# Optimization experiments

Measured on AMD Instinct MI355X. Metric: run time of the kernel, lower is better.

The kernel has to match this reference:

```python
import jax, jax.numpy as jnp
import numpy as np

NUM_JOINTS = 140
NUM_VERTICES = 13059
NUM_BONES = 28
BATCH = 512


def euler_zyx_to_rot(e):
    """e: [..., 3] Euler angles in (z, y, x) order -> [..., 3, 3] with R = Rz @ Ry @ Rx."""
    z, y, x = e[..., 0], e[..., 1], e[..., 2]
    cx, sx = jnp.cos(x), jnp.sin(x)
    cy, sy = jnp.cos(y), jnp.sin(y)
    cz, sz = jnp.cos(z), jnp.sin(z)
    r00 = cz * cy
    r01 = cz * sy * sx - sz * cx
    r02 = cz * sy * cx + sz * sx
    r10 = sz * cy
    r11 = sz * sy * sx + cz * cx
    r12 = sz * sy * cx - cz * sx
    r20 = -sy
    r21 = cy * sx
    r22 = cy * cx
    R = jnp.stack([r00, r01, r02, r10, r11, r12, r20, r21, r22], axis=-1)
    return R.reshape(e.shape[:-1] + (3, 3))


def _mouse_forward(pose, bone_lengths, center_bone_length, trans, scale,
                   v_template, t_pose_joints, weights, parent, bone_mapper):
    B = pose.shape[0]
    Jn = NUM_JOINTS
    dt = pose.dtype

    bl = jax.nn.sigmoid(bone_lengths / 5.0) * 2.0            # [B, 28]
    R = euler_zyx_to_rot(pose.reshape(B, Jn, 3))             # [B, J, 3, 3]
    Jt = t_pose_joints                                       # [J, 3]

    # bone offsets for joints 1..J-1, scaled per bone_length_mapper
    off = Jt[1:] - Jt[parent[1:]]                            # [J-1, 3]
    blid = bone_mapper[1:]                                   # [J-1]
    bl_g = jnp.where(blid[None, :] >= 0,
                     jnp.take(bl, jnp.maximum(blid, 0), axis=1),
                     jnp.ones((), dt))                       # [B, J-1]
    # joint index 1 (position 0 in the [J-1] arrays) uses center_bone_length
    scale_per = bl_g.at[:, 0].set(center_bone_length[:, 0])
    off_b = off[None] * scale_per[..., None]                 # [B, J-1, 3]

    bottom = jnp.broadcast_to(jnp.array([0., 0., 0., 1.], dt), (B, Jn - 1, 1, 4))
    top = jnp.concatenate([R[:, 1:], off_b[..., None]], axis=-1)   # [B, J-1, 3, 4]
    A = jnp.concatenate([top, bottom], axis=-2)              # [B, J-1, 4, 4] local transforms

    root_t = jnp.broadcast_to(Jt[0], (B, 3))[..., None]      # [B, 3, 1]
    root_top = jnp.concatenate([R[:, 0], root_t], axis=-1)   # [B, 3, 4]
    root_bot = jnp.broadcast_to(jnp.array([0., 0., 0., 1.], dt), (B, 1, 4))
    G0 = jnp.concatenate([root_top, root_bot], axis=-2)      # [B, 4, 4]

    G_init = jnp.zeros((B, Jn, 4, 4), dt).at[:, 0].set(G0)

    def step(G, xs):
        i, p, Ai = xs                                        # Ai: [B, 4, 4]
        Gp = jnp.take(G, p, axis=1)                          # [B, 4, 4]
        Gi = Gp @ Ai
        return G.at[:, i].set(Gi), None

    idx = jnp.arange(1, Jn)
    G, _ = jax.lax.scan(step, G_init, (idx, parent[1:], jnp.swapaxes(A, 0, 1)))

    J_final = G[:, :, :3, 3]                                 # [B, J, 3]

    # subtract rest-pose joint contribution (relative transforms for LBS)
    Jh = jnp.concatenate([jnp.broadcast_to(Jt, (B, Jn, 3)),
                          jnp.zeros((B, Jn, 1), dt)], axis=-1)      # [B, J, 4]
    d = jnp.einsum('bjmn,bjn->bjm', G, Jh)                   # [B, J, 4]
    G_rel = jnp.concatenate([G[..., :3], (G[..., 3] - d)[..., None]], axis=-1)

    # linear blend skinning
    T = jnp.einsum('vj,bjmn->bvmn', weights, G_rel)          # [B, V, 4, 4]
    vh = jnp.concatenate([v_template, jnp.ones((NUM_VERTICES, 1), dt)], axis=-1)
    V = jnp.einsum('bvmn,vn->bvm', T[:, :, :3, :], vh)       # [B, V, 3]

    s = scale[:, 0][:, None, None]
    V = V * s + trans[:, None, :]
    J_out = J_final * s + trans[:, None, :]
    return V, J_out


def setup_inputs() -> dict:
    key = jax.random.key(0)
    ks = jax.random.split(key, 8)
    rng = np.random.default_rng(0)
    parent = np.zeros(NUM_JOINTS, dtype=np.int32)
    for i in range(1, NUM_JOINTS):
        parent[i] = rng.integers(0, i)                       # valid kinematic tree
    bone_mapper = rng.integers(-1, NUM_BONES, size=NUM_JOINTS).astype(np.int32)
    W = jax.random.uniform(ks[6], (NUM_VERTICES, NUM_JOINTS), jnp.float32)
    W = W / jnp.sum(W, axis=1, keepdims=True)                # row-stochastic skinning weights
    return {
        'pose': jax.random.normal(ks[0], (BATCH, NUM_JOINTS * 3), jnp.float32) * 0.2,
        'bone_lengths': jax.random.normal(ks[1], (BATCH, NUM_BONES), jnp.float32),
        'center_bone_length': jax.random.uniform(ks[2], (BATCH, 1), jnp.float32, 0.5, 1.5),
        'trans': jax.random.normal(ks[3], (BATCH, 3), jnp.float32),
        'scale': jax.random.uniform(ks[4], (BATCH, 1), jnp.float32, 0.5, 1.5),
        'v_template': jax.random.normal(ks[5], (NUM_VERTICES, 3), jnp.float32),
        't_pose_joints': jax.random.normal(ks[7], (NUM_JOINTS, 3), jnp.float32),
        'weights': W,
        'parent': jnp.asarray(parent),
        'bone_mapper': jnp.asarray(bone_mapper),
    }


def reference(pose, bone_lengths, center_bone_length, trans, scale,
              v_template, t_pose_joints, weights, parent, bone_mapper):
    return _mouse_forward(pose, bone_lengths, center_bone_length, trans, scale,
                          v_template, t_pose_joints, weights, parent, bone_mapper)
```

## Files before the change

kernel.cpp:

```cpp
#include <hip/hip_runtime.h>
#include <math.h>

#define NJ 140
#define NV 13059
#define NB 512
#define NBONES 28

#define MTILES 103
#define NBLK 12
#define KS 18
#define GRID_GEMM (MTILES*NBLK)

#define APREP_SLOTS (MTILES*KS*512)

typedef _Float16 f16x8 __attribute__((ext_vector_type(8)));
typedef float    f32x4 __attribute__((ext_vector_type(4)));

#define GL16(gp, lp) __builtin_amdgcn_global_load_lds( \
    (const __attribute__((address_space(1))) unsigned int*)(gp), \
    (__attribute__((address_space(3))) unsigned int*)(lp), 16, 0, 0)

__global__ __launch_bounds__(256) void kin_kernel(
    const float* __restrict__ pose,
    const float* __restrict__ bone_lengths,
    const float* __restrict__ cbl,
    const float* __restrict__ trans,
    const float* __restrict__ scale,
    const float* __restrict__ t_pose,
    const int*   __restrict__ parent,
    const int*   __restrict__ bone_mapper,
    _Float16* __restrict__ Bp,
    float* __restrict__ jout)
{
    const int t = threadIdx.x;

    __shared__ float M0[NJ][12];
    __shared__ float M1[NJ][12];
    __shared__ int   a0[NJ];
    __shared__ int   a1[NJ];

    const int b = blockIdx.x;

    if (t < NJ) {
        const int j = t;
        float z = pose[b*(NJ*3) + 3*j + 0];
        float y = pose[b*(NJ*3) + 3*j + 1];
        float x = pose[b*(NJ*3) + 3*j + 2];
        float cx = cosf(x), sx = sinf(x);
        float cy = cosf(y), sy = sinf(y);
        float cz = cosf(z), sz = sinf(z);
        float r00 = cz*cy;
        float r01 = cz*sy*sx - sz*cx;
        float r02 = cz*sy*cx + sz*sx;
        float r10 = sz*cy;
        float r11 = sz*sy*sx + cz*cx;
        float r12 = sz*sy*cx - cz*sx;
        float r20 = -sy;
        float r21 = cy*sx;
        float r22 = cy*cx;
        float t0, t1, t2;
        int p = parent[j];
        if (j == 0) {
            t0 = t_pose[0]; t1 = t_pose[1]; t2 = t_pose[2];
        } else {
            float ox = t_pose[3*j+0] - t_pose[3*p+0];
            float oy = t_pose[3*j+1] - t_pose[3*p+1];
            float oz = t_pose[3*j+2] - t_pose[3*p+2];
            float s;
            if (j == 1) {
                s = cbl[b];
            } else {
                int blid = bone_mapper[j];
                if (blid >= 0) {
                    float bv = bone_lengths[b*NBONES + blid];
                    s = 2.0f / (1.0f + expf(-bv*0.2f));
                } else {
                    s = 1.0f;
                }
            }
            t0 = ox*s; t1 = oy*s; t2 = oz*s;
        }
        M0[j][0]=r00; M0[j][1]=r01; M0[j][2]=r02;  M0[j][3]=t0;
        M0[j][4]=r10; M0[j][5]=r11; M0[j][6]=r12;  M0[j][7]=t1;
        M0[j][8]=r20; M0[j][9]=r21; M0[j][10]=r22; M0[j][11]=t2;
        a0[j] = (j == 0) ? -1 : p;
    }
    __syncthreads();

    float* src = &M0[0][0]; float* dst = &M1[0][0];
    int* as = a0; int* ad = a1;
    for (int r = 0; r < 8; ++r) {
        if (t < NJ) {
            int a = as[t];
            const float* Mi = src + t*12;
            float* Do = dst + t*12;
            if (a >= 0) {
                const float* Mp = src + a*12;
                #pragma unroll
                for (int m = 0; m < 3; ++m) {
                    float p0 = Mp[m*4+0], p1 = Mp[m*4+1], p2 = Mp[m*4+2], p3 = Mp[m*4+3];
                    Do[m*4+0] = p0*Mi[0] + p1*Mi[4] + p2*Mi[8];
                    Do[m*4+1] = p0*Mi[1] + p1*Mi[5] + p2*Mi[9];
                    Do[m*4+2] = p0*Mi[2] + p1*Mi[6] + p2*Mi[10];
                    Do[m*4+3] = p0*Mi[3] + p1*Mi[7] + p2*Mi[11] + p3;
                }
                ad[t] = as[a];
            } else {
                #pragma unroll
                for (int e = 0; e < 12; ++e) Do[e] = Mi[e];
                ad[t] = -1;
            }
        }
        __syncthreads();
        float* tf = src; src = dst; dst = tf;
        int* ti = as; as = ad; ad = ti;
    }

    float* grl = dst;
    if (t < NJ) {
        const int j = t;
        const float* G = src + j*12;
        float sb = scale[b];
        float tr0 = trans[b*3+0], tr1 = trans[b*3+1], tr2 = trans[b*3+2];
        float* jo = jout + ((size_t)b*NJ + j)*3;
        jo[0] = G[3]*sb  + tr0;
        jo[1] = G[7]*sb  + tr1;
        jo[2] = G[11]*sb + tr2;
        float jx = t_pose[3*j+0], jy = t_pose[3*j+1], jz = t_pose[3*j+2];
        #pragma unroll
        for (int c = 0; c < 3; ++c) {
            float g0 = G[c*4+0], g1 = G[c*4+1], g2 = G[c*4+2];
            float g3 = G[c*4+3] - (g0*jx + g1*jy + g2*jz);
            grl[j*12 + c*4 + 0] = g0;
            grl[j*12 + c*4 + 1] = g1;
            grl[j*12 + c*4 + 2] = g2;
            grl[j*12 + c*4 + 3] = g3;
        }
    }
    __syncthreads();

    if (t < 216) {
        int c  = t / 72;
        int rr = t - c*72;
        int ks = rr >> 2;
        int ci = rr & 3;
        int nrow = b*3 + c;
        int nb = nrow >> 7;
        int rl = nrow & 127;
        int j0 = ks*8 + ci*2;
        f16x8 o;
        #pragma unroll
        for (int i = 0; i < 8; ++i) o[i] = (_Float16)0.f;
        if (j0 < NJ) {
            o[0] = (_Float16)grl[j0*12 + c*4 + 0];
            o[1] = (_Float16)grl[j0*12 + c*4 + 1];
            o[2] = (_Float16)grl[j0*12 + c*4 + 2];
            o[3] = (_Float16)grl[j0*12 + c*4 + 3];
        }
        if (j0 + 1 < NJ) {
            o[4] = (_Float16)grl[(j0+1)*12 + c*4 + 0];
            o[5] = (_Float16)grl[(j0+1)*12 + c*4 + 1];
            o[6] = (_Float16)grl[(j0+1)*12 + c*4 + 2];
            o[7] = (_Float16)grl[(j0+1)*12 + c*4 + 3];
        }
        int cs = ci ^ ((rl >> 1) & 3);
        *(f16x8*)(Bp + ((size_t)(nb*KS + ks)*512 + rl*4 + cs)*8) = o;
    }
}

__global__ __launch_bounds__(256) void aprep_kernel(
    const float* __restrict__ v_template,
    const float* __restrict__ weights,
    _Float16* __restrict__ Ap)
{
    const int t   = threadIdx.x;
    const int mt  = blockIdx.x / KS;
    const int ks  = blockIdx.x - mt*KS;
    const int row = t >> 1;
    const int q   = t & 1;
    const int v   = mt*128 + row;
    const int j0  = ks*8 + q*4;
    const int s   = (row >> 1) & 3;

    f16x8 oA, oB;
    #pragma unroll
    for (int i = 0; i < 8; ++i) { oA[i] = (_Float16)0.f; oB[i] = (_Float16)0.f; }

    if (v < NV && j0 + 3 < NJ) {
        float x = v_template[v*3+0];
        float y = v_template[v*3+1];
        float z = v_template[v*3+2];
        const float4 w4 = *(const float4*)(weights + (size_t)v*NJ + j0);
        oA[0] = (_Float16)(w4.x*x); oA[1] = (_Float16)(w4.x*y);
        oA[2] = (_Float16)(w4.x*z); oA[3] = (_Float16)w4.x;
        oA[4] = (_Float16)(w4.y*x); oA[5] = (_Float16)(w4.y*y);
        oA[6] = (_Float16)(w4.y*z); oA[7] = (_Float16)w4.y;
        oB[0] = (_Float16)(w4.z*x); oB[1] = (_Float16)(w4.z*y);
        oB[2] = (_Float16)(w4.z*z); oB[3] = (_Float16)w4.z;
        oB[4] = (_Float16)(w4.w*x); oB[5] = (_Float16)(w4.w*y);
        oB[6] = (_Float16)(w4.w*z); oB[7] = (_Float16)w4.w;
    }

    const int base = ((2*q) ^ s) & ~1;
    _Float16* dst = Ap + (((size_t)blockIdx.x)*512 + row*4 + base)*8;
    if (s & 1) {
        *(f16x8*)dst       = oB;
        *(f16x8*)(dst + 8) = oA;
    } else {
        *(f16x8*)dst       = oA;
        *(f16x8*)(dst + 8) = oB;
    }
}

__global__ __launch_bounds__(256) void gemm_kernel(
    const _Float16* __restrict__ Ap,
    const _Float16* __restrict__ Bp,
    const float* __restrict__ scale,
    const float* __restrict__ trans,
    float* __restrict__ vout)
{
    __shared__ _Float16 sA[3][4096];
    __shared__ _Float16 sB[3][4096];

    const int t    = threadIdx.x;
    const int lane = t & 63;
    const int wid  = t >> 6;
    const int ln   = lane & 15;
    const int kq   = lane >> 4;
    const int wm   = wid & 1;
    const int wn   = wid >> 1;

    const int q8 = GRID_GEMM >> 3;
    const int r8 = GRID_GEMM & 7;
    const int xcd = blockIdx.x & 7;
    const int idx = blockIdx.x >> 3;
    const int wgid = (xcd < r8 ? xcd*(q8+1) : r8*(q8+1) + (xcd-r8)*q8) + idx;

    const int mt = wgid / NBLK;
    const int nb = wgid - mt*NBLK;

    const _Float16* Ag = Ap + (size_t)mt*(KS*4096);
    const _Float16* Bg = Bp + (size_t)nb*(KS*4096);

    const int c1 = wid*64 + lane;
    const int c2 = c1 + 256;
    const int lb1 = wid*512;
    const int lb2 = 2048 + wid*512;

    const int csl = kq ^ ((ln >> 1) & 3);
    const int rA  = wm*64 + ln;
    const int rB  = wn*64 + ln;
    const int afo = rA*32 + csl*8;
    const int bfo = rB*32 + csl*8;

    f32x4 acc[4][4];
    #pragma unroll
    for (int mi = 0; mi < 4; ++mi)
        #pragma unroll
        for (int ni = 0; ni < 4; ++ni)
            acc[mi][ni] = (f32x4){0.f, 0.f, 0.f, 0.f};

    auto stage = [&](int buf, int ks) {
        const _Float16* a = Ag + ks*4096;
        const _Float16* b = Bg + ks*4096;
        GL16(a + c1*8, &sA[buf][lb1]);
        GL16(a + c2*8, &sA[buf][lb2]);
        GL16(b + c1*8, &sB[buf][lb1]);
        GL16(b + c2*8, &sB[buf][lb2]);
    };
    auto compute = [&](int buf) {
        f16x8 af[4], bf[4];
        #pragma unroll
        for (int mi = 0; mi < 4; ++mi)
            af[mi] = *(const f16x8*)&sA[buf][afo + mi*512];
        #pragma unroll
        for (int ni = 0; ni < 4; ++ni)
            bf[ni] = *(const f16x8*)&sB[buf][bfo + ni*512];
        #pragma unroll
        for (int mi = 0; mi < 4; ++mi)
            #pragma unroll
            for (int ni = 0; ni < 4; ++ni)
                acc[mi][ni] = __builtin_amdgcn_mfma_f32_16x16x32_f16(
                    af[mi], bf[ni], acc[mi][ni], 0, 0, 0);
    };

    #define WAITBAR4 do { \
        asm volatile("s_waitcnt vmcnt(4)" ::: "memory"); \
        __builtin_amdgcn_s_barrier(); } while (0)

    stage(0, 0);
    stage(1, 1);
    #pragma unroll 1
    for (int ks = 0; ks < KS - 3; ks += 3) {
        WAITBAR4; stage(2, ks + 2); compute(0);
        WAITBAR4; stage(0, ks + 3); compute(1);
        WAITBAR4; stage(1, ks + 4); compute(2);
    }
    WAITBAR4; stage(2, 17); compute(0);
    WAITBAR4; compute(1);
    asm volatile("s_waitcnt vmcnt(0)" ::: "memory");
    __builtin_amdgcn_s_barrier();
    compute(2);
    #undef WAITBAR4

    long long obase[4]; float es[4], etr[4];
    #pragma unroll
    for (int ni = 0; ni < 4; ++ni) {
        int n  = nb*128 + wn*64 + ni*16 + ln;
        int bq = n / 3;
        int cr = n - bq*3;
        obase[ni] = (long long)bq*(NV*3) + cr;
        es[ni]  = scale[bq];
        etr[ni] = trans[n];
    }
    const int vb = mt*128 + wm*64 + kq*4;
    #pragma unroll
    for (int mi = 0; mi < 4; ++mi) {
        #pragma unroll
        for (int ni = 0; ni < 4; ++ni) {
            #pragma unroll
            for (int r = 0; r < 4; ++r) {
                int vg = vb + mi*16 + r;
                if (vg < NV)
                    vout[obase[ni] + (long long)vg*3] =
                        acc[mi][ni][r]*es[ni] + etr[ni];
            }
        }
    }
}

extern "C" void kernel_launch(void* const* d_in, const int* in_sizes, int n_in,
                              void* d_out, int out_size, void* d_ws, size_t ws_size,
                              hipStream_t stream) {
    const float* pose         = (const float*)d_in[0];
    const float* bone_lengths = (const float*)d_in[1];
    const float* cbl          = (const float*)d_in[2];
    const float* trans        = (const float*)d_in[3];
    const float* scale        = (const float*)d_in[4];
    const float* v_template   = (const float*)d_in[5];
    const float* t_pose       = (const float*)d_in[6];
    const float* weights      = (const float*)d_in[7];
    const int*   parent       = (const int*)d_in[8];
    const int*   bone_mapper  = (const int*)d_in[9];

    float* vout = (float*)d_out;
    float* jout = vout + (size_t)NB*NV*3;

    _Float16* Ap = (_Float16*)d_ws;
    _Float16* Bp = Ap + (size_t)APREP_SLOTS*8;

    aprep_kernel<<<MTILES*KS, 256, 0, stream>>>(v_template, weights, Ap);
    kin_kernel<<<NB, 256, 0, stream>>>(
        pose, bone_lengths, cbl, trans, scale, t_pose,
        parent, bone_mapper, Bp, jout);
    gemm_kernel<<<GRID_GEMM, 256, 0, stream>>>(Ap, Bp, scale, trans, vout);
}
```

Baseline: 179.0 us.

## Merge prep kernels and load GEMM fragments directly into registers

The A-prep and kinematics kernels are merged into one launch, with blocks split by index, which removes one kernel launch and lets the two run at the same time. The GEMM drops its LDS triple-buffer staging through global_load_lds and barriers. Each wave now loads its MFMA fragments straight from global memory into a three-deep register ring, and the XOR swizzle in the packed layouts is removed to match. This trades LDS traffic and barriers for more VGPR pressure and uncoalesced, duplicated global loads, since A and B fragments are reread by multiple waves.

Result: slower. 194.1 us (+8.4%).

```diff
diff --git a/kernel.cpp b/kernel.cpp
--- a/kernel.cpp
+++ b/kernel.cpp
@@ -16,23 +16,55 @@
 typedef _Float16 f16x8 __attribute__((ext_vector_type(8)));
 typedef float    f32x4 __attribute__((ext_vector_type(4)));
 
-#define GL16(gp, lp) __builtin_amdgcn_global_load_lds( \
-    (const __attribute__((address_space(1))) unsigned int*)(gp), \
-    (__attribute__((address_space(3))) unsigned int*)(lp), 16, 0, 0)
-
-__global__ __launch_bounds__(256) void kin_kernel(
+__global__ __launch_bounds__(256) void prep_kernel(
     const float* __restrict__ pose,
     const float* __restrict__ bone_lengths,
     const float* __restrict__ cbl,
     const float* __restrict__ trans,
     const float* __restrict__ scale,
+    const float* __restrict__ v_template,
     const float* __restrict__ t_pose,
     const int*   __restrict__ parent,
     const int*   __restrict__ bone_mapper,
+    const float* __restrict__ weights,
+    _Float16* __restrict__ Ap,
     _Float16* __restrict__ Bp,
     float* __restrict__ jout)
 {
     const int t = threadIdx.x;
+
+    if (blockIdx.x >= NB) {
+        const int id  = blockIdx.x - NB;
+        const int mt  = id / KS;
+        const int ks  = id - mt*KS;
+        const int row = t >> 1;
+        const int q   = t & 1;
+        const int v   = mt*128 + row;
+        const int j0  = ks*8 + q*4;
+
+        f16x8 oA, oB;
+        #pragma unroll
+        for (int i = 0; i < 8; ++i) { oA[i] = (_Float16)0.f; oB[i] = (_Float16)0.f; }
+
+        if (v < NV && j0 + 3 < NJ) {
+            float x = v_template[v*3+0];
+            float y = v_template[v*3+1];
+            float z = v_template[v*3+2];
+            const float4 w4 = *(const float4*)(weights + (size_t)v*NJ + j0);
+            oA[0] = (_Float16)(w4.x*x); oA[1] = (_Float16)(w4.x*y);
+            oA[2] = (_Float16)(w4.x*z); oA[3] = (_Float16)w4.x;
+            oA[4] = (_Float16)(w4.y*x); oA[5] = (_Float16)(w4.y*y);
+            oA[6] = (_Float16)(w4.y*z); oA[7] = (_Float16)w4.y;
+            oB[0] = (_Float16)(w4.z*x); oB[1] = (_Float16)(w4.z*y);
+            oB[2] = (_Float16)(w4.z*z); oB[3] = (_Float16)w4.z;
+            oB[4] = (_Float16)(w4.w*x); oB[5] = (_Float16)(w4.w*y);
+            oB[6] = (_Float16)(w4.w*z); oB[7] = (_Float16)w4.w;
+        }
+        _Float16* dst = Ap + (((size_t)id)*512 + row*4 + 2*q)*8;
+        *(f16x8*)dst       = oA;
+        *(f16x8*)(dst + 8) = oB;
+        return;
+    }
 
     __shared__ float M0[NJ][12];
     __shared__ float M1[NJ][12];
@@ -145,7 +177,7 @@
         int ks = rr >> 2;
         int ci = rr & 3;
         int nrow = b*3 + c;
-        int nb = nrow >> 7;
+        int nbp = nrow >> 7;
         int rl = nrow & 127;
         int j0 = ks*8 + ci*2;
         f16x8 o;
@@ -163,52 +195,7 @@
             o[6] = (_Float16)grl[(j0+1)*12 + c*4 + 2];
             o[7] = (_Float16)grl[(j0+1)*12 + c*4 + 3];
         }
-        int cs = ci ^ ((rl >> 1) & 3);
-        *(f16x8*)(Bp + ((size_t)(nb*KS + ks)*512 + rl*4 + cs)*8) = o;
-    }
-}
-
-__global__ __launch_bounds__(256) void aprep_kernel(
-    const float* __restrict__ v_template,
-    const float* __restrict__ weights,
-    _Float16* __restrict__ Ap)
-{
-    const int t   = threadIdx.x;
-    const int mt  = blockIdx.x / KS;
-    const int ks  = blockIdx.x - mt*KS;
-    const int row = t >> 1;
-    const int q   = t & 1;
-    const int v   = mt*128 + row;
-    const int j0  = ks*8 + q*4;
-    const int s   = (row >> 1) & 3;
-
-    f16x8 oA, oB;
-    #pragma unroll
-    for (int i = 0; i < 8; ++i) { oA[i] = (_Float16)0.f; oB[i] = (_Float16)0.f; }
-
-    if (v < NV && j0 + 3 < NJ) {
-        float x = v_template[v*3+0];
-        float y = v_template[v*3+1];
-        float z = v_template[v*3+2];
-        const float4 w4 = *(const float4*)(weights + (size_t)v*NJ + j0);
-        oA[0] = (_Float16)(w4.x*x); oA[1] = (_Float16)(w4.x*y);
-        oA[2] = (_Float16)(w4.x*z); oA[3] = (_Float16)w4.x;
-        oA[4] = (_Float16)(w4.y*x); oA[5] = (_Float16)(w4.y*y);
-        oA[6] = (_Float16)(w4.y*z); oA[7] = (_Float16)w4.y;
-        oB[0] = (_Float16)(w4.z*x); oB[1] = (_Float16)(w4.z*y);
-        oB[2] = (_Float16)(w4.z*z); oB[3] = (_Float16)w4.z;
-        oB[4] = (_Float16)(w4.w*x); oB[5] = (_Float16)(w4.w*y);
-        oB[6] = (_Float16)(w4.w*z); oB[7] = (_Float16)w4.w;
-    }
-
-    const int base = ((2*q) ^ s) & ~1;
-    _Float16* dst = Ap + (((size_t)blockIdx.x)*512 + row*4 + base)*8;
-    if (s & 1) {
-        *(f16x8*)dst       = oB;
-        *(f16x8*)(dst + 8) = oA;
-    } else {
-        *(f16x8*)dst       = oA;
-        *(f16x8*)(dst + 8) = oB;
+        *(f16x8*)(Bp + ((size_t)(nbp*KS + ks)*512 + rl*4 + ci)*8) = o;
     }
 }
 
@@ -219,9 +206,6 @@
     const float* __restrict__ trans,
     float* __restrict__ vout)
 {
-    __shared__ _Float16 sA[3][4096];
-    __shared__ _Float16 sB[3][4096];
-
     const int t    = threadIdx.x;
     const int lane = t & 63;
     const int wid  = t >> 6;
@@ -239,19 +223,8 @@
     const int mt = wgid / NBLK;
     const int nb = wgid - mt*NBLK;
 
-    const _Float16* Ag = Ap + (size_t)mt*(KS*4096);
-    const _Float16* Bg = Bp + (size_t)nb*(KS*4096);
-
-    const int c1 = wid*64 + lane;
-    const int c2 = c1 + 256;
-    const int lb1 = wid*512;
-    const int lb2 = 2048 + wid*512;
-
-    const int csl = kq ^ ((ln >> 1) & 3);
-    const int rA  = wm*64 + ln;
-    const int rB  = wn*64 + ln;
-    const int afo = rA*32 + csl*8;
-    const int bfo = rB*32 + csl*8;
+    const _Float16* Ag = Ap + (size_t)mt*(KS*4096) + ((wm*64 + ln)*4 + kq)*8;
+    const _Float16* Bg = Bp + (size_t)nb*(KS*4096) + ((wn*64 + ln)*4 + kq)*8;
 
     f32x4 acc[4][4];
     #pragma unroll
@@ -260,48 +233,35 @@
         for (int ni = 0; ni < 4; ++ni)
             acc[mi][ni] = (f32x4){0.f, 0.f, 0.f, 0.f};
 
-    auto stage = [&](int buf, int ks) {
-        const _Float16* a = Ag + ks*4096;
-        const _Float16* b = Bg + ks*4096;
-        GL16(a + c1*8, &sA[buf][lb1]);
-        GL16(a + c2*8, &sA[buf][lb2]);
-        GL16(b + c1*8, &sB[buf][lb1]);
-        GL16(b + c2*8, &sB[buf][lb2]);
-    };
-    auto compute = [&](int buf) {
-        f16x8 af[4], bf[4];
-        #pragma unroll
-        for (int mi = 0; mi < 4; ++mi)
-            af[mi] = *(const f16x8*)&sA[buf][afo + mi*512];
-        #pragma unroll
-        for (int ni = 0; ni < 4; ++ni)
-            bf[ni] = *(const f16x8*)&sB[buf][bfo + ni*512];
-        #pragma unroll
-        for (int mi = 0; mi < 4; ++mi)
-            #pragma unroll
-            for (int ni = 0; ni < 4; ++ni)
-                acc[mi][ni] = __builtin_amdgcn_mfma_f32_16x16x32_f16(
-                    af[mi], bf[ni], acc[mi][ni], 0, 0, 0);
-    };
-
-    #define WAITBAR4 do { \
-        asm volatile("s_waitcnt vmcnt(4)" ::: "memory"); \
-        __builtin_amdgcn_s_barrier(); } while (0)
-
-    stage(0, 0);
-    stage(1, 1);
-    #pragma unroll 1
-    for (int ks = 0; ks < KS - 3; ks += 3) {
-        WAITBAR4; stage(2, ks + 2); compute(0);
-        WAITBAR4; stage(0, ks + 3); compute(1);
-        WAITBAR4; stage(1, ks + 4); compute(2);
-    }
-    WAITBAR4; stage(2, 17); compute(0);
-    WAITBAR4; compute(1);
-    asm volatile("s_waitcnt vmcnt(0)" ::: "memory");
-    __builtin_amdgcn_s_barrier();
-    compute(2);
-    #undef WAITBAR4
+    f16x8 af[3][4], bf[3][4];
+
+    #define LF(s, ksv) do { \
+        const _Float16* a_ = Ag + (ksv)*4096; \
+        const _Float16* b_ = Bg + (ksv)*4096; \
+        _Pragma("unroll") \
+        for (int mi = 0; mi < 4; ++mi) af[s][mi] = *(const f16x8*)(a_ + mi*512); \
+        _Pragma("unroll") \
+        for (int ni = 0; ni < 4; ++ni) bf[s][ni] = *(const f16x8*)(b_ + ni*512); \
+    } while (0)
+
+    #define CM(s) do { \
+        _Pragma("unroll") \
+        for (int mi = 0; mi < 4; ++mi) \
+            _Pragma("unroll") \
+            for (int ni = 0; ni < 4; ++ni) \
+                acc[mi][ni] = __builtin_amdgcn_mfma_f32_16x16x32_f16( \
+                    af[s][mi], bf[s][ni], acc[mi][ni], 0, 0, 0); \
+    } while (0)
+
+    LF(0, 0); LF(1, 1); LF(2, 2);
+    #pragma unroll
+    for (int ks = 0; ks < KS; ks += 3) {
+        CM(0); if (ks + 3 < KS) LF(0, ks + 3);
+        CM(1); if (ks + 4 < KS) LF(1, ks + 4);
+        CM(2); if (ks + 5 < KS) LF(2, ks + 5);
+    }
+    #undef LF
+    #undef CM
 
     long long obase[4]; float es[4], etr[4];
     #pragma unroll
@@ -349,9 +309,9 @@
     _Float16* Ap = (_Float16*)d_ws;
     _Float16* Bp = Ap + (size_t)APREP_SLOTS*8;
 
-    aprep_kernel<<<MTILES*KS, 256, 0, stream>>>(v_template, weights, Ap);
-    kin_kernel<<<NB, 256, 0, stream>>>(
-        pose, bone_lengths, cbl, trans, scale, t_pose,
-        parent, bone_mapper, Bp, jout);
+    prep_kernel<<<NB + MTILES*KS, 256, 0, stream>>>(
+        pose, bone_lengths, cbl, trans, scale, v_template, t_pose,
+        parent, bone_mapper, weights, Ap, Bp, jout);
+
     gemm_kernel<<<GRID_GEMM, 256, 0, stream>>>(Ap, Bp, scale, trans, vout);
 }
```

## Merge prep kernels into one launch and switch GEMM to double buffering

Applied to the files above, without the earlier changes.

Folds the A-operand prep kernel into the kinematics kernel as extra blocks, saving one kernel launch and letting the two prep workloads run concurrently. The GEMM drops from a triple-buffered LDS pipeline with explicit vmcnt waits to a double-buffered loop with __syncthreads, and adds a launch-bounds hint of 4 blocks per CU. Halving the LDS footprint is meant to raise occupancy. The trade-off is less prefetch depth and full barriers that wait on all outstanding loads, which can expose memory latency.

New measurement: 171.8 us. -4.0%, faster.

```diff
diff --git a/kernel.cpp b/kernel.cpp
--- a/kernel.cpp
+++ b/kernel.cpp
@@ -20,19 +20,62 @@
     (const __attribute__((address_space(1))) unsigned int*)(gp), \
     (__attribute__((address_space(3))) unsigned int*)(lp), 16, 0, 0)
 
-__global__ __launch_bounds__(256) void kin_kernel(
+__global__ __launch_bounds__(256) void prep_kernel(
     const float* __restrict__ pose,
     const float* __restrict__ bone_lengths,
     const float* __restrict__ cbl,
     const float* __restrict__ trans,
     const float* __restrict__ scale,
+    const float* __restrict__ v_template,
     const float* __restrict__ t_pose,
     const int*   __restrict__ parent,
     const int*   __restrict__ bone_mapper,
+    const float* __restrict__ weights,
+    _Float16* __restrict__ Ap,
     _Float16* __restrict__ Bp,
     float* __restrict__ jout)
 {
     const int t = threadIdx.x;
+
+    if (blockIdx.x >= NB) {
+        const int id  = blockIdx.x - NB;
+        const int mt  = id / KS;
+        const int ks  = id - mt*KS;
+        const int row = t >> 1;
+        const int q   = t & 1;
+        const int v   = mt*128 + row;
+        const int j0  = ks*8 + q*4;
+        const int s   = (row >> 1) & 3;
+
+        f16x8 oA, oB;
+        #pragma unroll
+        for (int i = 0; i < 8; ++i) { oA[i] = (_Float16)0.f; oB[i] = (_Float16)0.f; }
+
+        if (v < NV && j0 + 3 < NJ) {
+            float x = v_template[v*3+0];
+            float y = v_template[v*3+1];
+            float z = v_template[v*3+2];
+            const float4 w4 = *(const float4*)(weights + (size_t)v*NJ + j0);
+            oA[0] = (_Float16)(w4.x*x); oA[1] = (_Float16)(w4.x*y);
+            oA[2] = (_Float16)(w4.x*z); oA[3] = (_Float16)w4.x;
+            oA[4] = (_Float16)(w4.y*x); oA[5] = (_Float16)(w4.y*y);
+            oA[6] = (_Float16)(w4.y*z); oA[7] = (_Float16)w4.y;
+            oB[0] = (_Float16)(w4.z*x); oB[1] = (_Float16)(w4.z*y);
+            oB[2] = (_Float16)(w4.z*z); oB[3] = (_Float16)w4.z;
+            oB[4] = (_Float16)(w4.w*x); oB[5] = (_Float16)(w4.w*y);
+            oB[6] = (_Float16)(w4.w*z); oB[7] = (_Float16)w4.w;
+        }
+        const int base = ((2*q) ^ s) & ~1;
+        _Float16* dst = Ap + (((size_t)id)*512 + row*4 + base)*8;
+        if (s & 1) {
+            *(f16x8*)dst       = oB;
+            *(f16x8*)(dst + 8) = oA;
+        } else {
+            *(f16x8*)dst       = oA;
+            *(f16x8*)(dst + 8) = oB;
+        }
+        return;
+    }
 
     __shared__ float M0[NJ][12];
     __shared__ float M1[NJ][12];
@@ -145,7 +188,7 @@
         int ks = rr >> 2;
         int ci = rr & 3;
         int nrow = b*3 + c;
-        int nb = nrow >> 7;
+        int nbp = nrow >> 7;
         int rl = nrow & 127;
         int j0 = ks*8 + ci*2;
         f16x8 o;
@@ -164,63 +207,19 @@
             o[7] = (_Float16)grl[(j0+1)*12 + c*4 + 3];
         }
         int cs = ci ^ ((rl >> 1) & 3);
-        *(f16x8*)(Bp + ((size_t)(nb*KS + ks)*512 + rl*4 + cs)*8) = o;
+        *(f16x8*)(Bp + ((size_t)(nbp*KS + ks)*512 + rl*4 + cs)*8) = o;
     }
 }
 
-__global__ __launch_bounds__(256) void aprep_kernel(
-    const float* __restrict__ v_template,
-    const float* __restrict__ weights,
-    _Float16* __restrict__ Ap)
-{
-    const int t   = threadIdx.x;
-    const int mt  = blockIdx.x / KS;
-    const int ks  = blockIdx.x - mt*KS;
-    const int row = t >> 1;
-    const int q   = t & 1;
-    const int v   = mt*128 + row;
-    const int j0  = ks*8 + q*4;
-    const int s   = (row >> 1) & 3;
-
-    f16x8 oA, oB;
-    #pragma unroll
-    for (int i = 0; i < 8; ++i) { oA[i] = (_Float16)0.f; oB[i] = (_Float16)0.f; }
-
-    if (v < NV && j0 + 3 < NJ) {
-        float x = v_template[v*3+0];
-        float y = v_template[v*3+1];
-        float z = v_template[v*3+2];
-        const float4 w4 = *(const float4*)(weights + (size_t)v*NJ + j0);
-        oA[0] = (_Float16)(w4.x*x); oA[1] = (_Float16)(w4.x*y);
-        oA[2] = (_Float16)(w4.x*z); oA[3] = (_Float16)w4.x;
-        oA[4] = (_Float16)(w4.y*x); oA[5] = (_Float16)(w4.y*y);
-        oA[6] = (_Float16)(w4.y*z); oA[7] = (_Float16)w4.y;
-        oB[0] = (_Float16)(w4.z*x); oB[1] = (_Float16)(w4.z*y);
-        oB[2] = (_Float16)(w4.z*z); oB[3] = (_Float16)w4.z;
-        oB[4] = (_Float16)(w4.w*x); oB[5] = (_Float16)(w4.w*y);
-        oB[6] = (_Float16)(w4.w*z); oB[7] = (_Float16)w4.w;
-    }
-
-    const int base = ((2*q) ^ s) & ~1;
-    _Float16* dst = Ap + (((size_t)blockIdx.x)*512 + row*4 + base)*8;
-    if (s & 1) {
-        *(f16x8*)dst       = oB;
-        *(f16x8*)(dst + 8) = oA;
-    } else {
-        *(f16x8*)dst       = oA;
-        *(f16x8*)(dst + 8) = oB;
-    }
-}
-
-__global__ __launch_bounds__(256) void gemm_kernel(
+__global__ __launch_bounds__(256, 4) void gemm_kernel(
     const _Float16* __restrict__ Ap,
     const _Float16* __restrict__ Bp,
     const float* __restrict__ scale,
     const float* __restrict__ trans,
     float* __restrict__ vout)
 {
-    __shared__ _Float16 sA[3][4096];
-    __shared__ _Float16 sB[3][4096];
+    __shared__ _Float16 sA[2][4096];
+    __shared__ _Float16 sB[2][4096];
 
     const int t    = threadIdx.x;
     const int lane = t & 63;
@@ -284,24 +283,16 @@
                     af[mi], bf[ni], acc[mi][ni], 0, 0, 0);
     };
 
-    #define WAITBAR4 do { \
-        asm volatile("s_waitcnt vmcnt(4)" ::: "memory"); \
-        __builtin_amdgcn_s_barrier(); } while (0)
-
     stage(0, 0);
-    stage(1, 1);
     #pragma unroll 1
-    for (int ks = 0; ks < KS - 3; ks += 3) {
-        WAITBAR4; stage(2, ks + 2); compute(0);
-        WAITBAR4; stage(0, ks + 3); compute(1);
-        WAITBAR4; stage(1, ks + 4); compute(2);
-    }
-    WAITBAR4; stage(2, 17); compute(0);
-    WAITBAR4; compute(1);
-    asm volatile("s_waitcnt vmcnt(0)" ::: "memory");
-    __builtin_amdgcn_s_barrier();
-    compute(2);
-    #undef WAITBAR4
+    for (int ks = 0; ks < KS; ks += 2) {
+        __syncthreads();
+        if (ks + 1 < KS) stage(1, ks + 1);
+        compute(0);
+        __syncthreads();
+        if (ks + 2 < KS) stage(0, ks + 2);
+        compute(1);
+    }
 
     long long obase[4]; float es[4], etr[4];
     #pragma unroll
@@ -349,9 +340,9 @@
     _Float16* Ap = (_Float16*)d_ws;
     _Float16* Bp = Ap + (size_t)APREP_SLOTS*8;
 
-    aprep_kernel<<<MTILES*KS, 256, 0, stream>>>(v_template, weights, Ap);
-    kin_kernel<<<NB, 256, 0, stream>>>(
-        pose, bone_lengths, cbl, trans, scale, t_pose,
-        parent, bone_mapper, Bp, jout);
+    prep_kernel<<<NB + MTILES*KS, 256, 0, stream>>>(
+        pose, bone_lengths, cbl, trans, scale, v_template, t_pose,
+        parent, bone_mapper, weights, Ap, Bp, jout);
+
     gemm_kernel<<<GRID_GEMM, 256, 0, stream>>>(Ap, Bp, scale, trans, vout);
 }
```
